# Performance work log

Hardware: AMD Instinct MI355X
Metric: run time of the kernel (lower is better)

## Reference

```python
import jax, jax.numpy as jnp
import numpy as np

E = 1024
H = 16
F = 4096
B, S = 4, 2048
LN_EPS = 1e-5


def setup_inputs() -> dict:
    key = jax.random.key(0)
    ks = jax.random.split(key, 12)
    sE = 1.0 / np.sqrt(E)
    sF = 1.0 / np.sqrt(F)
    return {
        "x": jax.random.normal(ks[0], (B, S, E), dtype=jnp.float32),
        # attention projections (torch Linear weight layout [out,in], bias=False)
        "Wq": jax.random.uniform(ks[1], (E, E), jnp.float32, -sE, sE),
        "Wk": jax.random.uniform(ks[2], (E, E), jnp.float32, -sE, sE),
        "Wv": jax.random.uniform(ks[3], (E, E), jnp.float32, -sE, sE),
        "Wo": jax.random.uniform(ks[4], (E, E), jnp.float32, -sE, sE),
        # LayerNorms
        "g1": jnp.ones((E,), jnp.float32),
        "b1": jnp.zeros((E,), jnp.float32),
        "g2": jnp.ones((E,), jnp.float32),
        "b2": jnp.zeros((E,), jnp.float32),
        # FFN (classical): linear1 [F,E], linear2 [E,F]
        "W1": jax.random.uniform(ks[5], (F, E), jnp.float32, -sE, sE),
        "bb1": jax.random.uniform(ks[6], (F,), jnp.float32, -sE, sE),
        "W2": jax.random.uniform(ks[7], (E, F), jnp.float32, -sF, sF),
        "bb2": jax.random.uniform(ks[8], (F,), jnp.float32, -sF, sF)[:E] * 0 + jax.random.uniform(ks[9], (E,), jnp.float32, -sF, sF),
    }


def _layernorm(x, g, b):
    mu = jnp.mean(x, axis=-1, keepdims=True)
    var = jnp.mean(jnp.square(x - mu), axis=-1, keepdims=True)
    return (x - mu) * jax.lax.rsqrt(var + LN_EPS) * g + b


def reference(x, Wq, Wk, Wv, Wo, g1, b1, g2, b2, W1, bb1, W2, bb2):
    b, s, _ = x.shape
    hd = E // H
    # projections: torch Linear is x @ W.T
    q = (x @ Wq.T).reshape(b, s, H, hd).transpose(0, 2, 1, 3)  # [B,H,S,hd]
    k = (x @ Wk.T).reshape(b, s, H, hd).transpose(0, 2, 1, 3)
    v = (x @ Wv.T).reshape(b, s, H, hd).transpose(0, 2, 1, 3)
    scores = jnp.einsum('bhqd,bhkd->bhqk', q, k) / jnp.sqrt(jnp.float32(hd))
    probs = jax.nn.softmax(scores, axis=-1)
    attn = jnp.einsum('bhqk,bhkd->bhqd', probs, v)
    attn = attn.transpose(0, 2, 1, 3).reshape(b, s, E)
    attn_out = attn @ Wo.T
    # residual + LN (dropout=0 / eval)
    h = _layernorm(x + attn_out, g1, b1)
    # FFN
    ffn = jax.nn.relu(h @ W1.T + bb1) @ W2.T + bb2
    return _layernorm(h + ffn, g2, b2)
```

## Files before the change

### kernel.cpp

```cpp
#include <hip/hip_runtime.h>
#include <stdint.h>

#define E_DIM   1024
#define H_NUM   16
#define HD      64
#define F_DIM   4096
#define B_NUM   4
#define S_LEN   2048
#define M_ROWS  (B_NUM * S_LEN)
#define QKV_LD  3072

typedef unsigned short u16;
typedef __bf16 bf16_t;
typedef bf16_t  bf16x8 __attribute__((ext_vector_type(8)));
typedef u16     u16x8  __attribute__((ext_vector_type(8)));
typedef float   f32x4  __attribute__((ext_vector_type(4)));
typedef float   f32x16 __attribute__((ext_vector_type(16)));
typedef unsigned u32x4 __attribute__((ext_vector_type(4)));

#define AS1 __attribute__((address_space(1)))
#define AS3 __attribute__((address_space(3)))

__device__ __forceinline__ void gload_lds16(const void* g, void* l) {
    __builtin_amdgcn_global_load_lds((AS1 void*)g, (AS3 void*)l, 16, 0, 0);
}

__device__ __forceinline__ u16 f2b(float f) {
    union { float f; unsigned u; } a; a.f = f;
    unsigned u = a.u + 0x7fffu + ((a.u >> 16) & 1u);
    return (u16)(u >> 16);
}
__device__ __forceinline__ float b2f(u16 v) {
    union { unsigned u; float f; } a; a.u = ((unsigned)v) << 16;
    return a.f;
}

__device__ __forceinline__ unsigned cvt_pk_bf16(float lo, float hi) {
    unsigned r;
    asm("v_cvt_pk_bf16_f32 %0, %1, %2" : "=v"(r) : "v"(lo), "v"(hi));
    return r;
}

__device__ __forceinline__ int swz_c(int row) {
    return ((row & 7) << 4) ^ ((row & 8) << 2);
}
__device__ __forceinline__ int swz8(int row) {
    return (row & 7) << 4;
}

#define VM_WAIT(n) asm volatile("s_waitcnt vmcnt(" #n ")" ::: "memory")
#define SC_LOG2E 0.1803368801111204f

struct CastArgs {
    const float* src[7];
    u16* dst[7];
    float scale[7];
    unsigned cum4[8];
};

__global__ __launch_bounds__(256) void cast_multi(CastArgs a) {
    const int total = a.cum4[7];
    const int stride = gridDim.x * blockDim.x;
    for (int i = blockIdx.x * blockDim.x + threadIdx.x; i < total; i += stride) {
        int s = 0;
#pragma unroll
        for (int k = 1; k < 7; ++k) s += (i >= (int)a.cum4[k]);
        const int off = i - (int)a.cum4[s];
        const float sc = a.scale[s];
        float4 v = reinterpret_cast<const float4*>(a.src[s])[off];
        ushort4 o;
        o.x = f2b(v.x * sc); o.y = f2b(v.y * sc); o.z = f2b(v.z * sc); o.w = f2b(v.w * sc);
        reinterpret_cast<ushort4*>(a.dst[s])[off] = o;
    }
}

__device__ __forceinline__ void store_c(float* C, size_t idx, float v) { C[idx] = v; }
__device__ __forceinline__ void store_c(u16* C, size_t idx, float v)   { C[idx] = f2b(v); }

template <typename OutT, bool RELU, bool HASBIAS, int K, bool VSPLIT>
__global__ __launch_bounds__(256, 2)
void gemm2n(const u16* __restrict__ A, const u16* __restrict__ B,
            OutT* __restrict__ C, const float* __restrict__ bias,
            char* __restrict__ VtG, int M, int N) {
    constexpr int NT = K / 32;
    __shared__ __align__(16) char smem[3 * 24576];

    const int tid  = threadIdx.x;
    const int lane = tid & 63, wave = tid >> 6;
    const int lr   = lane & 15, kh = lane >> 4;
    const int wr   = wave >> 1, wc = wave & 1;

    const int nwg = gridDim.x * gridDim.y;
    int wg = blockIdx.y * gridDim.x + blockIdx.x;
    const int cpx = nwg >> 3;
    wg = (wg & 7) * cpx + (wg >> 3);
    const int bx = wg % gridDim.x, by = wg / gridDim.x;
    const int row0 = by * 256, col0 = bx * 128;

    const int srow = tid >> 2, scolb = (tid & 3) * 16;
    const char* Ag = (const char*)(A + (size_t)(row0 + srow) * K) + scolb;
    const char* Bg = (const char*)(B + (size_t)(col0 + srow) * K) + scolb;
    const size_t rstep = (size_t)64 * K * 2;

    auto stage = [&](int t) {
        char* s = smem + (t % 3) * 24576;
        const size_t ko = (size_t)t * 64;
#pragma unroll
        for (int r = 0; r < 4; ++r)
            gload_lds16(Ag + r * rstep + ko, s + r * 4096 + tid * 16);
#pragma unroll
        for (int r = 0; r < 2; ++r)
            gload_lds16(Bg + r * rstep + ko, s + 16384 + r * 4096 + tid * 16);
    };

    f32x4 acc[8][4] = {};
    stage(0); stage(1);

    for (int t = 0; t < NT; ++t) {
        if (t + 1 < NT) VM_WAIT(6);
        else            VM_WAIT(0);
        __builtin_amdgcn_s_barrier();
        __builtin_amdgcn_sched_barrier(0);
        if (t + 2 < NT) stage(t + 2);

        const char* s = smem + (t % 3) * 24576;
        bf16x8 af[8], bf[4];
#pragma unroll
        for (int m = 0; m < 8; ++m)
            af[m] = *(const bf16x8*)(s + (wr * 128 + m * 16 + lr) * 64 + kh * 16);
#pragma unroll
        for (int n = 0; n < 4; ++n)
            bf[n] = *(const bf16x8*)(s + 16384 + (wc * 64 + n * 16 + lr) * 64 + kh * 16);

        __builtin_amdgcn_s_setprio(1);
#pragma unroll
        for (int m = 0; m < 8; ++m)
#pragma unroll
            for (int n = 0; n < 4; ++n)
                acc[m][n] = __builtin_amdgcn_mfma_f32_16x16x32_bf16(af[m], bf[n], acc[m][n], 0, 0, 0);
        __builtin_amdgcn_s_setprio(0);
    }

    if (VSPLIT && col0 >= 2048) {
#pragma unroll
        for (int m = 0; m < 8; ++m) {
#pragma unroll
            for (int n = 0; n < 4; ++n) {
                const int colv = col0 - 2048 + wc * 64 + n * 16 + lr;
                const int h = colv >> 6, d = colv & 63;
                const int rowq = row0 + wr * 128 + m * 16 + kh * 4;
                const int bq = rowq >> 11, sq = rowq & 2047;
                const int kvt = sq >> 6, kl = sq & 63;
                const int g = kl >> 4, qb = kl & 12;
                const int slotq = ((qb & 4) << 1) | ((qb & 8) >> 1) | (qb & 3);
                const size_t byte_off = ((size_t)((bq * H_NUM + h) * HD + d) << 12)
                                        + kvt * 128 + ((((g << 4) + slotq) << 1) ^ swz8(d));
                const u16 p0 = f2b(acc[m][n][0]), p1 = f2b(acc[m][n][1]);
                const u16 p2 = f2b(acc[m][n][2]), p3 = f2b(acc[m][n][3]);
                uint2 pk;
                pk.x = (unsigned)p0 | ((unsigned)p1 << 16);
                pk.y = (unsigned)p2 | ((unsigned)p3 << 16);
                *(uint2*)(VtG + byte_off) = pk;
            }
        }
        return;
    }

#pragma unroll
    for (int m = 0; m < 8; ++m) {
#pragma unroll
        for (int n = 0; n < 4; ++n) {
            int col = col0 + wc * 64 + n * 16 + lr;
            float bv = 0.f;
            if constexpr (HASBIAS) bv = bias[col];
#pragma unroll
            for (int r = 0; r < 4; ++r) {
                int row = row0 + wr * 128 + m * 16 + kh * 4 + r;
                float v = acc[m][n][r] + bv;
                if constexpr (RELU) v = fmaxf(v, 0.f);
                store_c(C, (size_t)row * N + col, v);
            }
        }
    }
}

template <typename OutT, bool RELU, bool HASBIAS, int K>
__global__ __launch_bounds__(256, 3)
void gemm2h(const u16* __restrict__ A, const u16* __restrict__ B,
            OutT* __restrict__ C, const float* __restrict__ bias,
            int M, int N) {
    constexpr int NT = K / 32;
    __shared__ __align__(16) char smem[3 * 16384];

    const int tid  = threadIdx.x;
    const int lane = tid & 63, wave = tid >> 6;
    const int lr   = lane & 15, kh = lane >> 4;
    const int wr   = wave >> 1, wc = wave & 1;

    const int nwg = gridDim.x * gridDim.y;
    int wg = blockIdx.y * gridDim.x + blockIdx.x;
    const int cpx = nwg >> 3;
    wg = (wg & 7) * cpx + (wg >> 3);
    const int bx = wg % gridDim.x, by = wg / gridDim.x;
    const int row0 = by * 128, col0 = bx * 128;

    const int srow = tid >> 2;
    const int scolb = (tid & 3) * 16;
    const char* Ag = (const char*)(A + (size_t)(row0 + srow) * K) + scolb;
    const char* Bg = (const char*)(B + (size_t)(col0 + srow) * K) + scolb;
    const size_t rstep = (size_t)64 * K * 2;

    auto do_stage = [&](int t) {
        char* s = smem + (t % 3) * 16384;
        const size_t ko = (size_t)t * 64;
        gload_lds16(Ag + ko,         s + tid * 16);
        gload_lds16(Ag + rstep + ko, s + 4096 + tid * 16);
        gload_lds16(Bg + ko,         s + 8192 + tid * 16);
        gload_lds16(Bg + rstep + ko, s + 12288 + tid * 16);
    };

    f32x4 acc[4][4] = {};
    do_stage(0); do_stage(1);

    for (int t = 0; t < NT; ++t) {
        if (t + 1 < NT) VM_WAIT(4);
        else            VM_WAIT(0);
        __builtin_amdgcn_s_barrier();
        __builtin_amdgcn_sched_barrier(0);
        if (t + 2 < NT) do_stage(t + 2);

        const char* s = smem + (t % 3) * 16384;
        bf16x8 af[4], bf[4];
#pragma unroll
        for (int m = 0; m < 4; ++m)
            af[m] = *(const bf16x8*)(s + (wr * 64 + m * 16 + lr) * 64 + kh * 16);
#pragma unroll
        for (int n = 0; n < 4; ++n)
            bf[n] = *(const bf16x8*)(s + 8192 + (wc * 64 + n * 16 + lr) * 64 + kh * 16);

        __builtin_amdgcn_s_setprio(1);
#pragma unroll
        for (int m = 0; m < 4; ++m)
#pragma unroll
            for (int n = 0; n < 4; ++n)
                acc[m][n] = __builtin_amdgcn_mfma_f32_16x16x32_bf16(af[m], bf[n], acc[m][n], 0, 0, 0);
        __builtin_amdgcn_s_setprio(0);
    }

#pragma unroll
    for (int m = 0; m < 4; ++m) {
#pragma unroll
        for (int n = 0; n < 4; ++n) {
            int col = col0 + wc * 64 + n * 16 + lr;
            float bv = 0.f;
            if constexpr (HASBIAS) bv = bias[col];
#pragma unroll
            for (int r = 0; r < 4; ++r) {
                int row = row0 + wr * 64 + m * 16 + kh * 4 + r;
                float v = acc[m][n][r] + bv;
                if constexpr (RELU) v = fmaxf(v, 0.f);
                store_c(C, (size_t)row * N + col, v);
            }
        }
    }
}

__global__ __launch_bounds__(256, 4)
void attn_kernel(const u16* __restrict__ QKV, const char* __restrict__ VtG,
                 u16* __restrict__ Ob) {
    __shared__ char Ks[2][64 * 128];
    __shared__ char Vt[2][64 * 128];

    const int tid  = threadIdx.x;
    const int lane = tid & 63, wave = tid >> 6;
    const int l31  = lane & 31, hi = lane >> 5;
    const int q0   = blockIdx.x * 128;
    const int h    = blockIdx.y;
    const int b    = blockIdx.z;

    const u16* Q  = QKV;
    const u16* Kp = QKV + 1024;

    const size_t qrow = (size_t)(b * S_LEN + q0 + wave * 32 + l31);
    bf16x8 qf[4];
#pragma unroll
    for (int c = 0; c < 4; ++c)
        qf[c] = *(const bf16x8*)(Q + qrow * QKV_LD + h * HD + c * 16 + hi * 8);

    bf16x8 ones;
#pragma unroll
    for (int j = 0; j < 8; ++j) ones[j] = (bf16_t)1.0f;

    f32x16 o0 = {}, o1 = {}, accl = {};

    const char* Kg  = (const char*)(Kp + (size_t)(b * S_LEN) * QKV_LD + h * HD);
    const char* Vgb = VtG + ((size_t)((b * H_NUM + h) * HD) << 12);

    int st_row[2], st_colb[2], st_lds[2], kst_colb[2];
#pragma unroll
    for (int j = 0; j < 2; ++j) {
        const int ob = (wave * 2 + j) * 1024 + lane * 16;
        st_row[j]   = ob >> 7;
        st_colb[j]  = ob & 127;
        kst_colb[j] = (ob & 127) ^ swz_c(st_row[j]);
        st_lds[j]   = (wave * 2 + j) * 1024;
    }
    const int krd = l31 * 128;
    const int vrd = l31 * 128;

#pragma unroll
    for (int j = 0; j < 2; ++j) {
        gload_lds16(Kg + (size_t)st_row[j] * (QKV_LD * 2) + kst_colb[j], Ks[0] + st_lds[j]);
        gload_lds16(Vgb + (size_t)st_row[j] * 4096 + st_colb[j],         Vt[0] + st_lds[j]);
    }
    __syncthreads();

    const int NT = S_LEN / 64;
    for (int t = 0; t < NT; ++t) {
        const int cur = t & 1;
        if (t < NT - 1) {
            const int kv0n = (t + 1) * 64;
#pragma unroll
            for (int j = 0; j < 2; ++j) {
                gload_lds16(Kg + (size_t)(kv0n + st_row[j]) * (QKV_LD * 2) + kst_colb[j],
                            Ks[cur ^ 1] + st_lds[j]);
                gload_lds16(Vgb + (size_t)st_row[j] * 4096 + (t + 1) * 128 + st_colb[j],
                            Vt[cur ^ 1] + st_lds[j]);
            }
        }

#pragma unroll
        for (int half = 0; half < 2; ++half) {
            const char* ksb = Ks[cur] + half * 4096 + krd;
            f32x16 st = {};
#pragma unroll
            for (int c = 0; c < 4; ++c) {
                bf16x8 kf = *(const bf16x8*)(ksb + ((c * 32 + hi * 16) ^ swz_c(l31)));
                st = __builtin_amdgcn_mfma_f32_32x32x16_bf16(kf, qf[c], st, 0, 0, 0);
            }

#pragma unroll
            for (int i = 0; i < 16; ++i)
                st[i] = __builtin_amdgcn_exp2f(st[i]);

            unsigned w[8];
#pragma unroll
            for (int i = 0; i < 8; ++i) w[i] = cvt_pk_bf16(st[2 * i], st[2 * i + 1]);

#pragma unroll
            for (int cc = 0; cc < 2; ++cc) {
                u32x4 fw;
                fw[0] = w[4 * cc];     fw[1] = w[4 * cc + 1];
                fw[2] = w[4 * cc + 2]; fw[3] = w[4 * cc + 3];
                bf16x8 pf = __builtin_bit_cast(bf16x8, fw);
                const int colb = (half * 64 + cc * 32 + hi * 16) ^ swz8(l31);
                bf16x8 v0 = *(const bf16x8*)(Vt[cur] + vrd + colb);
                bf16x8 v1 = *(const bf16x8*)(Vt[cur] + 4096 + vrd + colb);
                o0   = __builtin_amdgcn_mfma_f32_32x32x16_bf16(v0, pf, o0, 0, 0, 0);
                o1   = __builtin_amdgcn_mfma_f32_32x32x16_bf16(v1, pf, o1, 0, 0, 0);
                accl = __builtin_amdgcn_mfma_f32_32x32x16_bf16(ones, pf, accl, 0, 0, 0);
            }
        }
        __syncthreads();
    }

    const float inv = 1.0f / accl[0];
    unsigned m0[16], xx[16];
#pragma unroll
    for (int g = 0; g < 4; ++g)
#pragma unroll
        for (int u = 0; u < 2; ++u) {
            int r = g * 4 + 2 * u;
            m0[2 * g + u]     = cvt_pk_bf16(o0[r] * inv, o0[r + 1] * inv);
            m0[8 + 2 * g + u] = cvt_pk_bf16(o1[r] * inv, o1[r + 1] * inv);
        }
#pragma unroll
    for (int i = 0; i < 16; ++i) xx[i] = __shfl_xor(m0[i], 32);

    {
        unsigned full[8], sec[8];
#pragma unroll
        for (int g = 0; g < 4; ++g) {
            full[2 * g + 0] = hi ? xx[8 + 2 * g]     : m0[2 * g];
            full[2 * g + 1] = hi ? xx[8 + 2 * g + 1] : m0[2 * g + 1];
            sec[2 * g + 0]  = hi ? m0[8 + 2 * g]     : xx[2 * g];
            sec[2 * g + 1]  = hi ? m0[8 + 2 * g + 1] : xx[2 * g + 1];
        }
        u32x4 out0, out1, out2, out3;
        out0[0] = full[0]; out0[1] = full[1]; out0[2] = sec[0]; out0[3] = sec[1];
        out1[0] = full[2]; out1[1] = full[3]; out1[2] = sec[2]; out1[3] = sec[3];
        out2[0] = full[4]; out2[1] = full[5]; out2[2] = sec[4]; out2[3] = sec[5];
        out3[0] = full[6]; out3[1] = full[7]; out3[2] = sec[6]; out3[3] = sec[7];
        u16* op = Ob + qrow * E_DIM + h * HD + hi * 32;
        *(u32x4*)(op)      = out0;
        *(u32x4*)(op + 8)  = out1;
        *(u32x4*)(op + 16) = out2;
        *(u32x4*)(op + 24) = out3;
    }
}

template <typename XA>
__device__ __forceinline__ float4 ld4(const XA* p, size_t idx) {
    if constexpr (sizeof(XA) == 2) {
        ushort4 v = reinterpret_cast<const ushort4*>(p)[idx];
        float4 o; o.x = b2f(v.x); o.y = b2f(v.y); o.z = b2f(v.z); o.w = b2f(v.w);
        return o;
    } else {
        return reinterpret_cast<const float4*>(p)[idx];
    }
}

template <typename XA, typename XB>
__global__ __launch_bounds__(256)
void add_ln(const XA* __restrict__ xa, const XB* __restrict__ xb2,
            const float* __restrict__ g, const float* __restrict__ be,
            float* __restrict__ of, u16* __restrict__ ob) {
    const int row = blockIdx.x;
    const int t = threadIdx.x;
    const int lane = t & 63, wave = t >> 6;

    float4 va = ld4<XA>(xa + (size_t)row * E_DIM, t);
    float4 vb = ld4<XB>(xb2 + (size_t)row * E_DIM, t);
    float v0 = va.x + vb.x, v1 = va.y + vb.y, v2 = va.z + vb.z, v3 = va.w + vb.w;
    float s  = v0 + v1 + v2 + v3;
    float s2 = v0 * v0 + v1 * v1 + v2 * v2 + v3 * v3;
#pragma unroll
    for (int m = 32; m >= 1; m >>= 1) {
        s  += __shfl_xor(s, m);
        s2 += __shfl_xor(s2, m);
    }
    __shared__ float red[8];
    if (lane == 0) { red[wave] = s; red[4 + wave] = s2; }
    __syncthreads();
    s  = red[0] + red[1] + red[2] + red[3];
    s2 = red[4] + red[5] + red[6] + red[7];

    float mu   = s * (1.0f / E_DIM);
    float var  = s2 * (1.0f / E_DIM) - mu * mu;
    float rstd = rsqrtf(var + 1e-5f);

    float4 gg = reinterpret_cast<const float4*>(g)[t];
    float4 bb = reinterpret_cast<const float4*>(be)[t];
    float y0 = (v0 - mu) * rstd * gg.x + bb.x;
    float y1 = (v1 - mu) * rstd * gg.y + bb.y;
    float y2 = (v2 - mu) * rstd * gg.z + bb.z;
    float y3 = (v3 - mu) * rstd * gg.w + bb.w;
    if (of) {
        float4 o; o.x = y0; o.y = y1; o.z = y2; o.w = y3;
        reinterpret_cast<float4*>(of + (size_t)row * E_DIM)[t] = o;
    }
    if (ob) {
        ushort4 o;
        o.x = f2b(y0); o.y = f2b(y1); o.z = f2b(y2); o.w = f2b(y3);
        reinterpret_cast<ushort4*>(ob + (size_t)row * E_DIM)[t] = o;
    }
}

extern "C" void kernel_launch(void* const* d_in, const int* in_sizes, int n_in,
                              void* d_out, int out_size, void* d_ws, size_t ws_size,
                              hipStream_t stream) {
    const float* x   = (const float*)d_in[0];
    const float* Wq  = (const float*)d_in[1];
    const float* Wk  = (const float*)d_in[2];
    const float* Wv  = (const float*)d_in[3];
    const float* Wo  = (const float*)d_in[4];
    const float* g1  = (const float*)d_in[5];
    const float* b1  = (const float*)d_in[6];
    const float* g2  = (const float*)d_in[7];
    const float* b2  = (const float*)d_in[8];
    const float* W1  = (const float*)d_in[9];
    const float* bb1 = (const float*)d_in[10];
    const float* W2  = (const float*)d_in[11];
    const float* bb2 = (const float*)d_in[12];
    float* out = (float*)d_out;

    char* ws = (char*)d_ws;
    const size_t MB = 1024ull * 1024ull;
    u16* wqkvb = (u16*)(ws + 0 * MB);
    u16* wob   = (u16*)(ws + 6 * MB);
    u16* w1b   = (u16*)(ws + 8 * MB);
    u16* w2b   = (u16*)(ws + 16 * MB);
    u16* xb    = (u16*)(ws + 24 * MB);
    u16* qkvb  = (u16*)(ws + 40 * MB);
    u16* attnb = (u16*)(ws + 88 * MB);
    u16* attno = (u16*)(ws + 104 * MB);
    u16* hb    = (u16*)(ws + 136 * MB);
    char* VtG  = (ws + 152 * MB);
    u16* ffn1  = (u16*)(ws + 24 * MB);
    u16* y2b   = (u16*)(ws + 104 * MB);

    dim3 blk(256);

    CastArgs ca;
    ca.src[0] = x;   ca.dst[0] = xb;                            ca.scale[0] = 1.f;
    ca.src[1] = Wq;  ca.dst[1] = wqkvb;                         ca.scale[1] = SC_LOG2E;
    ca.src[2] = Wk;  ca.dst[2] = wqkvb + E_DIM * E_DIM;         ca.scale[2] = 1.f;
    ca.src[3] = Wv;  ca.dst[3] = wqkvb + 2 * E_DIM * E_DIM;     ca.scale[3] = 1.f;
    ca.src[4] = Wo;  ca.dst[4] = wob;                           ca.scale[4] = 1.f;
    ca.src[5] = W1;  ca.dst[5] = w1b;                           ca.scale[5] = 1.f;
    ca.src[6] = W2;  ca.dst[6] = w2b;                           ca.scale[6] = 1.f;
    unsigned n4[7] = {M_ROWS * E_DIM / 4, E_DIM * E_DIM / 4, E_DIM * E_DIM / 4,
                      E_DIM * E_DIM / 4, E_DIM * E_DIM / 4, F_DIM * E_DIM / 4,
                      E_DIM * F_DIM / 4};
    ca.cum4[0] = 0;
    for (int i = 0; i < 7; ++i) ca.cum4[i + 1] = ca.cum4[i] + n4[i];
    cast_multi<<<dim3(2048), blk, 0, stream>>>(ca);

    gemm2n<u16, false, false, E_DIM, true><<<dim3(QKV_LD / 128, M_ROWS / 256), blk, 0, stream>>>(
        xb, wqkvb, qkvb, nullptr, VtG, M_ROWS, QKV_LD);

    attn_kernel<<<dim3(S_LEN / 128, H_NUM, B_NUM), blk, 0, stream>>>(qkvb, VtG, attnb);

    gemm2h<u16, false, false, E_DIM><<<dim3(E_DIM / 128, M_ROWS / 128), blk, 0, stream>>>(
        attnb, wob, attno, nullptr, M_ROWS, E_DIM);

    add_ln<u16, u16><<<dim3(M_ROWS), blk, 0, stream>>>(xb, attno, g1, b1, nullptr, hb);

    gemm2n<u16, true, true, E_DIM, false><<<dim3(F_DIM / 128, M_ROWS / 256), blk, 0, stream>>>(
        hb, w1b, ffn1, bb1, nullptr, M_ROWS, F_DIM);

    gemm2h<u16, false, true, F_DIM><<<dim3(E_DIM / 128, M_ROWS / 128), blk, 0, stream>>>(
        ffn1, w2b, y2b, bb2, M_ROWS, E_DIM);

    add_ln<u16, u16><<<dim3(M_ROWS), blk, 0, stream>>>(hb, y2b, g2, b2, out, nullptr);
}
```

Baseline: 361.3 us.

## Add 256x256 eight-wave pipelined GEMM kernel for FFN first layer

Adds a new GEMM kernel with 512 threads (8 waves) computing 256x256 output tiles with 64-wide K tiles, double-buffered in 128 KB of LDS via direct global-to-LDS loads. Staging of the next tiles is interleaved with the MFMA phases, with barriers and setprio used to overlap loads and compute. It replaces the 256x128 gemm2n for the FFN1 (ReLU+bias) GEMM to raise arithmetic intensity per byte loaded. The cost is one workgroup per CU at large register and LDS use, which lowers occupancy and leaves little room to hide latency.

```diff
diff --git a/kernel.cpp b/kernel.cpp
--- a/kernel.cpp
+++ b/kernel.cpp
@@ -76,6 +76,104 @@
 
 __device__ __forceinline__ void store_c(float* C, size_t idx, float v) { C[idx] = v; }
 __device__ __forceinline__ void store_c(u16* C, size_t idx, float v)   { C[idx] = f2b(v); }
+
+template <typename OutT, bool RELU, bool HASBIAS, int K>
+__global__ __launch_bounds__(512, 1)
+void gemm8p(const u16* __restrict__ A, const u16* __restrict__ B,
+            OutT* __restrict__ C, const float* __restrict__ bias,
+            int M, int N) {
+    constexpr int NKT = K / 64;
+    __shared__ __align__(16) char smem[131072];
+
+    const int tid  = threadIdx.x;
+    const int lane = tid & 63, wave = tid >> 6;
+    const int lr   = lane & 15, kh = lane >> 4;
+    const int wr   = wave >> 2, wc = wave & 3;
+
+    const int nwg = gridDim.x * gridDim.y;
+    int wg = blockIdx.y * gridDim.x + blockIdx.x;
+    const int cpx = nwg >> 3;
+    wg = (wg & 7) * cpx + (wg >> 3);
+    const int bx = wg % gridDim.x, by = wg / gridDim.x;
+    const int row0 = by * 256, col0 = bx * 256;
+
+    const int srow = tid >> 2, skb = (tid & 3) * 16;
+    const char* Ag = (const char*)(A + (size_t)(row0 + srow) * K) + skb;
+    const char* Bg = (const char*)(B + (size_t)(col0 + srow) * K) + skb;
+    const size_t rstep = (size_t)128 * K * 2;
+    char* dstb = smem + tid * 16;
+
+    auto stage = [&](int stile, int r) {
+        const char* g = (r < 2) ? Ag : Bg;
+        const size_t ko = (size_t)stile * 128 + (r & 1) * 64;
+        char* d = dstb + (stile & 1) * 65536 + r * 16384;
+        gload_lds16(g + ko,         d);
+        gload_lds16(g + rstep + ko, d + 8192);
+    };
+
+    f32x4 acc[8][4] = {};
+    bf16x8 bf[4];
+
+    stage(0, 0); stage(0, 1); stage(0, 2); stage(0, 3);
+    if (NKT > 1) { stage(1, 0); stage(1, 2); }
+    VM_WAIT(4);
+    __builtin_amdgcn_s_barrier();
+    __builtin_amdgcn_sched_barrier(0);
+
+    for (int kt = 0; kt < NKT; ++kt) {
+        const char* buf = smem + (kt & 1) * 65536;
+#pragma unroll
+        for (int j = 0; j < 4; ++j) {
+            const int ks = j >> 1, mh = j & 1;
+            bf16x8 af[4];
+            const char* ab = buf + ks * 16384 + (wr * 128 + mh * 64 + lr) * 64 + kh * 16;
+#pragma unroll
+            for (int mm = 0; mm < 4; ++mm) af[mm] = *(const bf16x8*)(ab + mm * 1024);
+            if (mh == 0) {
+                const char* bb = buf + 32768 + ks * 16384 + (wc * 64 + lr) * 64 + kh * 16;
+#pragma unroll
+                for (int n = 0; n < 4; ++n) bf[n] = *(const bf16x8*)(bb + n * 1024);
+            }
+            {
+                const int stile = (j < 2) ? kt + 1 : kt + 2;
+                const int sreg  = (j == 0) ? 1 : (j == 1) ? 3 : (j == 2) ? 0 : 2;
+                if (stile < NKT) stage(stile, sreg);
+            }
+            if (kt < NKT - 2 || (kt == NKT - 2 && j < 2)) { VM_WAIT(6); }
+            else                                          { VM_WAIT(0); }
+            __builtin_amdgcn_s_barrier();
+            asm volatile("s_waitcnt lgkmcnt(0)" ::: "memory");
+            __builtin_amdgcn_sched_barrier(0);
+            __builtin_amdgcn_s_setprio(1);
+#pragma unroll
+            for (int mm = 0; mm < 4; ++mm)
+#pragma unroll
+                for (int n = 0; n < 4; ++n)
+                    acc[mh * 4 + mm][n] =
+                        __builtin_amdgcn_mfma_f32_16x16x32_bf16(af[mm], bf[n], acc[mh * 4 + mm][n], 0, 0, 0);
+            __builtin_amdgcn_s_setprio(0);
+            __builtin_amdgcn_s_barrier();
+            __builtin_amdgcn_sched_barrier(0);
+        }
+    }
+
+#pragma unroll
+    for (int m = 0; m < 8; ++m) {
+#pragma unroll
+        for (int n = 0; n < 4; ++n) {
+            int col = col0 + wc * 64 + n * 16 + lr;
+            float bv = 0.f;
+            if constexpr (HASBIAS) bv = bias[col];
+#pragma unroll
+            for (int r = 0; r < 4; ++r) {
+                int row = row0 + wr * 128 + m * 16 + kh * 4 + r;
+                float v = acc[m][n][r] + bv;
+                if constexpr (RELU) v = fmaxf(v, 0.f);
+                store_c(C, (size_t)row * N + col, v);
+            }
+        }
+    }
+}
 
 template <typename OutT, bool RELU, bool HASBIAS, int K, bool VSPLIT>
 __global__ __launch_bounds__(256, 2)
@@ -516,8 +614,8 @@
 
     add_ln<u16, u16><<<dim3(M_ROWS), blk, 0, stream>>>(xb, attno, g1, b1, nullptr, hb);
 
-    gemm2n<u16, true, true, E_DIM, false><<<dim3(F_DIM / 128, M_ROWS / 256), blk, 0, stream>>>(
-        hb, w1b, ffn1, bb1, nullptr, M_ROWS, F_DIM);
+    gemm8p<u16, true, true, E_DIM><<<dim3(F_DIM / 256, M_ROWS / 256), dim3(512), 0, stream>>>(
+        hb, w1b, ffn1, bb1, M_ROWS, F_DIM);
 
     gemm2h<u16, false, true, F_DIM><<<dim3(E_DIM / 128, M_ROWS / 128), blk, 0, stream>>>(
         ffn1, w2b, y2b, bb2, M_ROWS, E_DIM);
```

New measurement: 364.2 us. No clear change (+0.8%).

## Use 512-thread attention blocks covering 256 queries with head-major grid order

Applied to the files above, without the earlier changes.

Attention blocks now have 8 waves covering 256 query rows, so each staged K/V tile in LDS is shared by twice as many queries and every thread issues one async load per tile instead of two. The grid is flattened to 512 blocks, with batch*head in the low bits so that consecutive blocks hit different heads. This halves K/V global traffic per query. The costs are fewer blocks (512) for filling the CUs and larger launch bounds that may constrain registers.

```diff
diff --git a/kernel.cpp b/kernel.cpp
--- a/kernel.cpp
+++ b/kernel.cpp
@@ -265,7 +265,7 @@
     }
 }
 
-__global__ __launch_bounds__(256, 4)
+__global__ __launch_bounds__(512, 4)
 void attn_kernel(const u16* __restrict__ QKV, const char* __restrict__ VtG,
                  u16* __restrict__ Ob) {
     __shared__ char Ks[2][64 * 128];
@@ -274,9 +274,11 @@
     const int tid  = threadIdx.x;
     const int lane = tid & 63, wave = tid >> 6;
     const int l31  = lane & 31, hi = lane >> 5;
-    const int q0   = blockIdx.x * 128;
-    const int h    = blockIdx.y;
-    const int b    = blockIdx.z;
+    const int bid  = blockIdx.x;
+    const int bh   = bid & 63;
+    const int q0   = (bid >> 6) * 256;
+    const int h    = bh & 15;
+    const int b    = bh >> 4;
 
     const u16* Q  = QKV;
     const u16* Kp = QKV + 1024;
@@ -296,23 +298,16 @@
     const char* Kg  = (const char*)(Kp + (size_t)(b * S_LEN) * QKV_LD + h * HD);
     const char* Vgb = VtG + ((size_t)((b * H_NUM + h) * HD) << 12);
 
-    int st_row[2], st_colb[2], st_lds[2], kst_colb[2];
-#pragma unroll
-    for (int j = 0; j < 2; ++j) {
-        const int ob = (wave * 2 + j) * 1024 + lane * 16;
-        st_row[j]   = ob >> 7;
-        st_colb[j]  = ob & 127;
-        kst_colb[j] = (ob & 127) ^ swz_c(st_row[j]);
-        st_lds[j]   = (wave * 2 + j) * 1024;
-    }
+    const int ob      = wave * 1024 + lane * 16;
+    const int st_row  = ob >> 7;
+    const int st_colb = ob & 127;
+    const int kst_colb = st_colb ^ swz_c(st_row);
+    const int st_lds  = wave * 1024;
     const int krd = l31 * 128;
     const int vrd = l31 * 128;
 
-#pragma unroll
-    for (int j = 0; j < 2; ++j) {
-        gload_lds16(Kg + (size_t)st_row[j] * (QKV_LD * 2) + kst_colb[j], Ks[0] + st_lds[j]);
-        gload_lds16(Vgb + (size_t)st_row[j] * 4096 + st_colb[j],         Vt[0] + st_lds[j]);
-    }
+    gload_lds16(Kg + (size_t)st_row * (QKV_LD * 2) + kst_colb, Ks[0] + st_lds);
+    gload_lds16(Vgb + (size_t)st_row * 4096 + st_colb,         Vt[0] + st_lds);
     __syncthreads();
 
     const int NT = S_LEN / 64;
@@ -320,13 +315,10 @@
         const int cur = t & 1;
         if (t < NT - 1) {
             const int kv0n = (t + 1) * 64;
-#pragma unroll
-            for (int j = 0; j < 2; ++j) {
-                gload_lds16(Kg + (size_t)(kv0n + st_row[j]) * (QKV_LD * 2) + kst_colb[j],
-                            Ks[cur ^ 1] + st_lds[j]);
-                gload_lds16(Vgb + (size_t)st_row[j] * 4096 + (t + 1) * 128 + st_colb[j],
-                            Vt[cur ^ 1] + st_lds[j]);
-            }
+            gload_lds16(Kg + (size_t)(kv0n + st_row) * (QKV_LD * 2) + kst_colb,
+                        Ks[cur ^ 1] + st_lds);
+            gload_lds16(Vgb + (size_t)st_row * 4096 + (t + 1) * 128 + st_colb,
+                        Vt[cur ^ 1] + st_lds);
         }
 
 #pragma unroll
@@ -509,7 +501,7 @@
     gemm2n<u16, false, false, E_DIM, true><<<dim3(QKV_LD / 128, M_ROWS / 256), blk, 0, stream>>>(
         xb, wqkvb, qkvb, nullptr, VtG, M_ROWS, QKV_LD);
 
-    attn_kernel<<<dim3(S_LEN / 128, H_NUM, B_NUM), blk, 0, stream>>>(qkvb, VtG, attnb);
+    attn_kernel<<<dim3(512), dim3(512), 0, stream>>>(qkvb, VtG, attnb);
 
     gemm2h<u16, false, false, E_DIM><<<dim3(E_DIM / 128, M_ROWS / 128), blk, 0, stream>>>(
         attnb, wob, attno, nullptr, M_ROWS, E_DIM);
```

Measured after the change: 350.0 us. -3.1%, faster.
